# Optimization experiments

Measured on AMD Instinct MI355X. Metric: run time of the kernel, lower is better.

The kernel has to match this reference:

```python
import jax, jax.numpy as jnp
import numpy as np

B, S, F = 512, 512, 128   # batch, seq_len, facts_size (= querry_size)
H1, H2 = 80, 40
PAD = float(-2**32 + 1)


def setup_inputs() -> dict:
    key = jax.random.key(0)
    ks = jax.random.split(key, 12)
    inp = {
        "query": jax.random.normal(ks[0], (B, F), jnp.float32),
        "facts": jax.random.normal(ks[1], (B, S, F), jnp.float32),
        "mask": jax.random.randint(ks[2], (B, S), 0, 2, jnp.int32),
        # mlp1: querry_size -> facts_size
        "W1": jax.random.normal(ks[3], (F, F), jnp.float32) / np.sqrt(F),
        "b1": jnp.zeros((F,), jnp.float32),
        # PReLU alpha (per-feature, init zeros)
        "alpha": jnp.zeros((F,), jnp.float32),
        # mlp2: 4*F -> 80
        "W2": jax.random.normal(ks[4], (4 * F, H1), jnp.float32) / np.sqrt(4 * F),
        "b2": jnp.zeros((H1,), jnp.float32),
        # mlp3: 80 -> 40
        "W3": jax.random.normal(ks[5], (H1, H2), jnp.float32) / np.sqrt(H1),
        "b3": jnp.zeros((H2,), jnp.float32),
        # mlp4: 40 -> 1
        "W4": jax.random.normal(ks[6], (H2, 1), jnp.float32) / np.sqrt(H2),
        "b4": jnp.zeros((1,), jnp.float32),
    }
    return inp


def reference(query, facts, mask, W1, b1, alpha, W2, b2, W3, b3, W4, b4):
    # mlp1 + PReLU on the query
    q = query @ W1 + b1                                   # [B, F]
    q = jnp.where(q >= 0, q, alpha * q)                   # PReLU, alpha per-feature
    # broadcast query over sequence (tile+reshape in the original)
    qs = jnp.broadcast_to(q[:, None, :], (q.shape[0], S, F))  # [B, S, F]
    din = jnp.concatenate([qs, facts, qs - facts, qs * facts], axis=-1)  # [B,S,4F]
    h1 = jax.nn.sigmoid(din @ W2 + b2)                    # [B, S, 80]
    h2 = jax.nn.sigmoid(h1 @ W3 + b3)                     # [B, S, 40]
    scores = (h2 @ W4 + b4)[..., 0][:, None, :]           # [B, 1, S]
    key_masks = (mask == 1)[:, None, :]                   # [B, 1, S]
    scores = jnp.where(key_masks, scores, PAD)
    scores = jax.nn.softmax(scores, axis=-1)              # softmax over seq
    out = jnp.einsum("bqs,bsf->bqf", scores, facts)       # [B, 1, F]  (mode SUM)
    return out
```

## Files before the change

kernel.cpp:

```cpp
#include <hip/hip_runtime.h>
#include <hip/hip_bf16.h>

typedef __bf16 bf16x8 __attribute__((ext_vector_type(8)));
typedef float  f32x4  __attribute__((ext_vector_type(4)));

#define WBT_STRIDE 136
#define H1_STRIDE  104
#define W3T_STRIDE 104

#define LOAD_TILE(av, tile)                                                     \
    {                                                                           \
        const float* p0 = &fb[(size_t)(wave * 64 + (tile) * 16 + m) * 128 + qd * 8]; \
        _Pragma("unroll")                                                       \
        for (int kc = 0; kc < 4; ++kc) {                                        \
            av[kc][0] = *(const f32x4*)(p0 + kc * 32);                          \
            av[kc][1] = *(const f32x4*)(p0 + kc * 32 + 4);                      \
        }                                                                       \
    }

#define TILE_BODY(av, mvv)                                                      \
    {                                                                           \
        bf16x8 af[4];                                                           \
        _Pragma("unroll")                                                       \
        for (int kc = 0; kc < 4; ++kc)                                          \
            _Pragma("unroll")                                                   \
            for (int i = 0; i < 8; ++i)                                         \
                af[kc][i] = (__bf16)((i < 4) ? av[kc][0][i] : av[kc][1][i - 4]);\
         \
        _Pragma("unroll")                                                       \
        for (int ct = 0; ct < 5; ++ct) {                                        \
            f32x4 acc = {0.f, 0.f, 0.f, 0.f};                                   \
            _Pragma("unroll")                                                   \
            for (int kc = 0; kc < 4; ++kc) {                                    \
                bf16x8 bfr = *(const bf16x8*)&WbT[(ct * 16 + m) * WBT_STRIDE + kc * 32 + qd * 8]; \
                acc = __builtin_amdgcn_mfma_f32_16x16x32_bf16(af[kc], bfr, acc, 0, 0, 0); \
            }                                                                   \
            const int col = ct * 16 + m;    \
            const float qc = qcs[col];                                          \
            _Pragma("unroll")                                                   \
            for (int r = 0; r < 4; ++r) {                                       \
                float x = acc[r] + qc;                                          \
                float h = __builtin_amdgcn_rcpf(1.0f + __expf(-x));             \
                h1w[(qd * 4 + r) * H1_STRIDE + col] = (__bf16)h;                \
            }                                                                   \
        }                                                                       \
        asm volatile("s_waitcnt lgkmcnt(0)" ::: "memory");    \
                      \
        bf16x8 a2[3];                                                           \
        _Pragma("unroll")                                                       \
        for (int kc = 0; kc < 3; ++kc)                                          \
            a2[kc] = *(const bf16x8*)&h1w[m * H1_STRIDE + kc * 32 + qd * 8];    \
        float sc[4] = {0.f, 0.f, 0.f, 0.f};                                     \
        _Pragma("unroll")                                                       \
        for (int ct = 0; ct < 3; ++ct) {                                        \
            f32x4 acc2 = {0.f, 0.f, 0.f, 0.f};                                  \
            _Pragma("unroll")                                                   \
            for (int kc = 0; kc < 3; ++kc) {                                    \
                bf16x8 bfr = *(const bf16x8*)&W3T[(ct * 16 + m) * W3T_STRIDE + kc * 32 + qd * 8]; \
                acc2 = __builtin_amdgcn_mfma_f32_16x16x32_bf16(a2[kc], bfr, acc2, 0, 0, 0); \
            }                                                                   \
            const int col = ct * 16 + m;                                        \
            const float w4v = w4s[col], b3v = b3s[col];                         \
            _Pragma("unroll")                                                   \
            for (int r = 0; r < 4; ++r) {                                       \
                float h2 = __builtin_amdgcn_rcpf(1.0f + __expf(-(acc2[r] + b3v))); \
                sc[r] = fmaf(h2, w4v, sc[r]);                                   \
            }                                                                   \
        }                                                                       \
        _Pragma("unroll")                                                       \
        for (int d = 1; d < 16; d <<= 1)                                        \
            _Pragma("unroll")                                                   \
            for (int r = 0; r < 4; ++r)                                         \
                sc[r] += __shfl_xor(sc[r], d);                                  \
          \
        float s0v = __int_as_float(__builtin_amdgcn_ds_bpermute(idx, __float_as_int(sc[0]))); \
        float s1v = __int_as_float(__builtin_amdgcn_ds_bpermute(idx, __float_as_int(sc[1]))); \
        float s2v = __int_as_float(__builtin_amdgcn_ds_bpermute(idx, __float_as_int(sc[2]))); \
        float s3v = __int_as_float(__builtin_amdgcn_ds_bpermute(idx, __float_as_int(sc[3]))); \
        const int rr = m & 3;                                                   \
        float srow = (rr == 0) ? s0v : (rr == 1) ? s1v : (rr == 2) ? s2v : s3v; \
               \
        const float pm = ((mvv) == 1) ? __expf(srow) : 0.f;                     \
        Zl += pm;                                                               \
        _Pragma("unroll")                                                       \
        for (int kc = 0; kc < 4; ++kc)                                          \
            _Pragma("unroll")                                                   \
            for (int i = 0; i < 4; ++i) {                                       \
                oacc[kc][i]     = fmaf(pm, av[kc][0][i], oacc[kc][i]);          \
                oacc[kc][i + 4] = fmaf(pm, av[kc][1][i], oacc[kc][i + 4]);      \
            }                                                                   \
    }

__global__ __launch_bounds__(512, 4)
void attn_fused(const float* __restrict__ query,
                const float* __restrict__ facts,
                const int*   __restrict__ mask,
                const float* __restrict__ W1, const float* __restrict__ b1,
                const float* __restrict__ alpha,
                const float* __restrict__ W2, const float* __restrict__ b2,
                const float* __restrict__ W3, const float* __restrict__ b3,
                const float* __restrict__ W4,
                float* __restrict__ out)
{
    __shared__ __align__(16) __bf16 WbT[80 * WBT_STRIDE];
    __shared__ __align__(16) __bf16 W3T[48 * W3T_STRIDE];
    __shared__ __align__(16) __bf16 h1all[128 * H1_STRIDE];
    __shared__ float qy[128], qs[128], qcs[80];
    __shared__ float qpart[4][128], qcp[4][80];
    __shared__ float w4s[48], b3s[48];
    __shared__ float outw[8 * 128];
    __shared__ float Zw[8];

    const int b = blockIdx.x, t = threadIdx.x;
    const int wave = t >> 6, lane = t & 63, qd = lane >> 4, m = lane & 15;
    const float* fb = facts + (size_t)b * (512 * 128);
    const int*   mb = mask + b * 512;

    f32x4 av0[4][2], av1[4][2];
    LOAD_TILE(av0, 0)
    LOAD_TILE(av1, 1)
    const int mv0 = mb[wave * 64 + m];
    const int mv1 = mb[wave * 64 + 16 + m];
    const int mv2 = mb[wave * 64 + 32 + m];
    const int mv3 = mb[wave * 64 + 48 + m];

    if (t < 128) qy[t] = query[b * 128 + t];
    for (int e = t; e < 48 * 96; e += 512) {
        int j = e / 96, k = e % 96;
        W3T[j * W3T_STRIDE + k] = (j < 40 && k < 80) ? (__bf16)W3[k * 40 + j]
                                                     : (__bf16)0.0f;
    }
    for (int e = t; e < 128 * 16; e += 512) {
        int r = e >> 4, c = 80 + (e & 15);
        h1all[r * H1_STRIDE + c] = (__bf16)0.0f;
    }
    if (t < 48) { w4s[t] = (t < 40) ? W4[t] : 0.f; b3s[t] = (t < 40) ? b3[t] : 0.f; }
    __syncthreads();

    {
        int j = t & 127, kh = t >> 7;
        float acc = (kh == 0) ? b1[j] : 0.f;
        const float* w1p = W1 + (kh * 32) * 128 + j;
        #pragma unroll 8
        for (int k = 0; k < 32; ++k) acc = fmaf(qy[kh * 32 + k], w1p[k * 128], acc);
        qpart[kh][j] = acc;
    }
    __syncthreads();
    if (t < 128) {
        float s = (qpart[0][t] + qpart[1][t]) + (qpart[2][t] + qpart[3][t]);
        qs[t] = (s >= 0.f) ? s : alpha[t] * s;
    }
    __syncthreads();

    if (t < 320) {
        int jj = t % 80, hh = t / 80;
        float acc = (hh == 0) ? b2[jj] : 0.f;
        #pragma unroll 8
        for (int k = hh * 32; k < hh * 32 + 32; ++k)
            acc = fmaf(qs[k], W2[k * 80 + jj] + W2[(256 + k) * 80 + jj], acc);
        qcp[hh][jj] = acc;
    }
    for (int e = t; e < 128 * 80; e += 512) {
        int k = e / 80, n = e - k * 80;
        float w = W2[(128 + k) * 80 + n] - W2[(256 + k) * 80 + n]
                + qs[k] * W2[(384 + k) * 80 + n];
        WbT[n * WBT_STRIDE + k] = (__bf16)w;
    }
    __syncthreads();
    if (t < 80) qcs[t] = (qcp[0][t] + qcp[1][t]) + (qcp[2][t] + qcp[3][t]);
    __syncthreads();

    __bf16* h1w = &h1all[wave * 16 * H1_STRIDE];
    const int idx = ((((m >> 2) << 4) | m) << 2);

    float oacc[4][8];
    #pragma unroll
    for (int kc = 0; kc < 4; ++kc)
        #pragma unroll
        for (int i = 0; i < 8; ++i) oacc[kc][i] = 0.f;
    float Zl = 0.f;

    TILE_BODY(av0, mv0)
    LOAD_TILE(av0, 2)
    TILE_BODY(av1, mv1)
    LOAD_TILE(av1, 3)
    TILE_BODY(av0, mv2)
    TILE_BODY(av1, mv3)

    #pragma unroll
    for (int d = 1; d < 16; d <<= 1) {
        #pragma unroll
        for (int kc = 0; kc < 4; ++kc)
            #pragma unroll
            for (int i = 0; i < 8; ++i)
                oacc[kc][i] += __shfl_xor(oacc[kc][i], d);
        Zl += __shfl_xor(Zl, d);
    }
    if (m == 0) {
        #pragma unroll
        for (int kc = 0; kc < 4; ++kc)
            #pragma unroll
            for (int i = 0; i < 8; ++i)
                outw[wave * 128 + kc * 32 + qd * 8 + i] = oacc[kc][i];
        if (lane == 0) Zw[wave] = Zl;
    }
    __syncthreads();

    if (t < 128) {
        float v = 0.f, Z = 0.f;
        #pragma unroll
        for (int w = 0; w < 8; ++w) { v += outw[w * 128 + t]; Z += Zw[w]; }
        out[b * 128 + t] = v / Z;
    }
}

extern "C" void kernel_launch(void* const* d_in, const int* in_sizes, int n_in,
                              void* d_out, int out_size, void* d_ws, size_t ws_size,
                              hipStream_t stream) {
    (void)in_sizes; (void)n_in; (void)d_ws; (void)ws_size; (void)out_size;
    const float* query = (const float*)d_in[0];
    const float* facts = (const float*)d_in[1];
    const int*   mask  = (const int*)d_in[2];
    const float* W1 = (const float*)d_in[3];
    const float* b1 = (const float*)d_in[4];
    const float* al = (const float*)d_in[5];
    const float* W2 = (const float*)d_in[6];
    const float* b2 = (const float*)d_in[7];
    const float* W3 = (const float*)d_in[8];
    const float* b3 = (const float*)d_in[9];
    const float* W4 = (const float*)d_in[10];
    const float* b4 = (const float*)d_in[11];
    (void)b4;
    attn_fused<<<dim3(512), dim3(512), 0, stream>>>(
        query, facts, mask, W1, b1, al, W2, b2, W3, b3, W4, (float*)d_out);
}
```

Before: 259.5 us.

## Split score computation from weighted accumulation to cut live registers

Each tile's fp32 facts are converted to bf16 and the scores are computed right away, before the output accumulators exist. All four tiles are then re-read from global memory in a second pass that does the weighted sum. This keeps the 32 oacc registers out of the MLP/MFMA phase so register pressure drops there, in exchange for loading the facts tiles twice (second read likely from cache).

```diff
diff --git a/kernel.cpp b/kernel.cpp
--- a/kernel.cpp
+++ b/kernel.cpp
@@ -18,14 +18,15 @@
         }                                                                       \
     }
 
-#define TILE_BODY(av, mvv)                                                      \
+#define CONV_AF(af, av)                                                         \
+    _Pragma("unroll")                                                           \
+    for (int kc = 0; kc < 4; ++kc)                                              \
+        _Pragma("unroll")                                                       \
+        for (int i = 0; i < 8; ++i)                                             \
+            af[kc][i] = (__bf16)((i < 4) ? av[kc][0][i] : av[kc][1][i - 4]);
+
+#define SCORE_TILE(af, mvv, pmv)                                                \
     {                                                                           \
-        bf16x8 af[4];                                                           \
-        _Pragma("unroll")                                                       \
-        for (int kc = 0; kc < 4; ++kc)                                          \
-            _Pragma("unroll")                                                   \
-            for (int i = 0; i < 8; ++i)                                         \
-                af[kc][i] = (__bf16)((i < 4) ? av[kc][0][i] : av[kc][1][i - 4]);\
          \
         _Pragma("unroll")                                                       \
         for (int ct = 0; ct < 5; ++ct) {                                        \
@@ -80,16 +81,18 @@
         const int rr = m & 3;                                                   \
         float srow = (rr == 0) ? s0v : (rr == 1) ? s1v : (rr == 2) ? s2v : s3v; \
                \
-        const float pm = ((mvv) == 1) ? __expf(srow) : 0.f;                     \
-        Zl += pm;                                                               \
-        _Pragma("unroll")                                                       \
-        for (int kc = 0; kc < 4; ++kc)                                          \
-            _Pragma("unroll")                                                   \
-            for (int i = 0; i < 4; ++i) {                                       \
-                oacc[kc][i]     = fmaf(pm, av[kc][0][i], oacc[kc][i]);          \
-                oacc[kc][i + 4] = fmaf(pm, av[kc][1][i], oacc[kc][i + 4]);      \
-            }                                                                   \
-    }
+        pmv = ((mvv) == 1) ? __expf(srow) : 0.f;                                \
+        Zl += pmv;                                                              \
+    }
+
+#define ACC_TILE(bv, pmv)                                                       \
+    _Pragma("unroll")                                                           \
+    for (int kc = 0; kc < 4; ++kc)                                              \
+        _Pragma("unroll")                                                       \
+        for (int i = 0; i < 4; ++i) {                                           \
+            oacc[kc][i]     = fmaf(pmv, bv[kc][0][i], oacc[kc][i]);             \
+            oacc[kc][i + 4] = fmaf(pmv, bv[kc][1][i], oacc[kc][i + 4]);         \
+        }
 
 __global__ __launch_bounds__(512, 4)
 void attn_fused(const float* __restrict__ query,
@@ -173,19 +176,38 @@
     __bf16* h1w = &h1all[wave * 16 * H1_STRIDE];
     const int idx = ((((m >> 2) << 4) | m) << 2);
 
+    float Zl = 0.f;
+    float pm0, pm1, pm2, pm3;
+    bf16x8 af[4];
+
+    CONV_AF(af, av0)
+    LOAD_TILE(av0, 2)
+    SCORE_TILE(af, mv0, pm0)
+
+    CONV_AF(af, av1)
+    LOAD_TILE(av1, 3)
+    SCORE_TILE(af, mv1, pm1)
+
+    CONV_AF(af, av0)
+    SCORE_TILE(af, mv2, pm2)
+
+    CONV_AF(af, av1)
+    SCORE_TILE(af, mv3, pm3)
+
     float oacc[4][8];
     #pragma unroll
     for (int kc = 0; kc < 4; ++kc)
         #pragma unroll
         for (int i = 0; i < 8; ++i) oacc[kc][i] = 0.f;
-    float Zl = 0.f;
-
-    TILE_BODY(av0, mv0)
+
+    LOAD_TILE(av0, 0)
+    LOAD_TILE(av1, 1)
+    ACC_TILE(av0, pm0)
     LOAD_TILE(av0, 2)
-    TILE_BODY(av1, mv1)
+    ACC_TILE(av1, pm1)
     LOAD_TILE(av1, 3)
-    TILE_BODY(av0, mv2)
-    TILE_BODY(av1, mv3)
+    ACC_TILE(av0, pm2)
+    ACC_TILE(av1, pm3)
 
     #pragma unroll
     for (int d = 1; d < 16; d <<= 1) {
```

After: 249.8 us. -3.7%, faster.

## Stage softmax weights in LDS and re-read facts for weighted sum

Applied to the files above, without the earlier changes.

Each tile now stores only its per-row softmax numerators in shared memory instead of accumulating a 32-float weighted-sum register array per lane. After scoring, each wave re-reads its 64 fact rows from global memory (L2 cache) with coalesced lane-per-column loads and accumulates the output directly. This removes the large cross-lane shuffle reduction of the output. Double-buffered register tiles are replaced by a single buffer that is prefetched one tile ahead, and the launch bound is relaxed to 2 blocks per CU. The aim is to cut register pressure and shuffle cost, at the price of a second pass over facts through cache and possibly lower occupancy.

```diff
diff --git a/kernel.cpp b/kernel.cpp
--- a/kernel.cpp
+++ b/kernel.cpp
@@ -18,14 +18,15 @@
         }                                                                       \
     }
 
-#define TILE_BODY(av, mvv)                                                      \
+#define CONV_AF(af, av)                                                         \
+    _Pragma("unroll")                                                           \
+    for (int kc = 0; kc < 4; ++kc)                                              \
+        _Pragma("unroll")                                                       \
+        for (int i = 0; i < 8; ++i)                                             \
+            af[kc][i] = (__bf16)((i < 4) ? av[kc][0][i] : av[kc][1][i - 4]);
+
+#define SCORE_TILE(af, mvv, tile)                                               \
     {                                                                           \
-        bf16x8 af[4];                                                           \
-        _Pragma("unroll")                                                       \
-        for (int kc = 0; kc < 4; ++kc)                                          \
-            _Pragma("unroll")                                                   \
-            for (int i = 0; i < 8; ++i)                                         \
-                af[kc][i] = (__bf16)((i < 4) ? av[kc][0][i] : av[kc][1][i - 4]);\
          \
         _Pragma("unroll")                                                       \
         for (int ct = 0; ct < 5; ++ct) {                                        \
@@ -80,18 +81,12 @@
         const int rr = m & 3;                                                   \
         float srow = (rr == 0) ? s0v : (rr == 1) ? s1v : (rr == 2) ? s2v : s3v; \
                \
-        const float pm = ((mvv) == 1) ? __expf(srow) : 0.f;                     \
-        Zl += pm;                                                               \
-        _Pragma("unroll")                                                       \
-        for (int kc = 0; kc < 4; ++kc)                                          \
-            _Pragma("unroll")                                                   \
-            for (int i = 0; i < 4; ++i) {                                       \
-                oacc[kc][i]     = fmaf(pm, av[kc][0][i], oacc[kc][i]);          \
-                oacc[kc][i + 4] = fmaf(pm, av[kc][1][i], oacc[kc][i + 4]);      \
-            }                                                                   \
-    }
-
-__global__ __launch_bounds__(512, 4)
+        const float pmv = ((mvv) == 1) ? __expf(srow) : 0.f;                    \
+        Zl += pmv;                                                              \
+        if (qd == 0) pmall[wave * 64 + (tile) * 16 + m] = pmv;                  \
+    }
+
+__global__ __launch_bounds__(512, 2)
 void attn_fused(const float* __restrict__ query,
                 const float* __restrict__ facts,
                 const int*   __restrict__ mask,
@@ -109,6 +104,7 @@
     __shared__ float qpart[4][128], qcp[4][80];
     __shared__ float w4s[48], b3s[48];
     __shared__ float outw[8 * 128];
+    __shared__ float pmall[8 * 64];
     __shared__ float Zw[8];
 
     const int b = blockIdx.x, t = threadIdx.x;
@@ -116,9 +112,8 @@
     const float* fb = facts + (size_t)b * (512 * 128);
     const int*   mb = mask + b * 512;
 
-    f32x4 av0[4][2], av1[4][2];
-    LOAD_TILE(av0, 0)
-    LOAD_TILE(av1, 1)
+    f32x4 av[4][2];
+    LOAD_TILE(av, 0)
     const int mv0 = mb[wave * 64 + m];
     const int mv1 = mb[wave * 64 + 16 + m];
     const int mv2 = mb[wave * 64 + 32 + m];
@@ -173,37 +168,42 @@
     __bf16* h1w = &h1all[wave * 16 * H1_STRIDE];
     const int idx = ((((m >> 2) << 4) | m) << 2);
 
-    float oacc[4][8];
+    float Zl = 0.f;
+    bf16x8 af[4];
+
+    CONV_AF(af, av)
+    LOAD_TILE(av, 1)
+    SCORE_TILE(af, mv0, 0)
+
+    CONV_AF(af, av)
+    LOAD_TILE(av, 2)
+    SCORE_TILE(af, mv1, 1)
+
+    CONV_AF(af, av)
+    LOAD_TILE(av, 3)
+    SCORE_TILE(af, mv2, 2)
+
+    CONV_AF(af, av)
+    SCORE_TILE(af, mv3, 3)
+
+    asm volatile("s_waitcnt lgkmcnt(0)" ::: "memory");
+    float oA = 0.f, oB = 0.f;
+    {
+        const float* fw = fb + (size_t)(wave * 64) * 128;
+        const float* pmw = &pmall[wave * 64];
+        #pragma unroll 8
+        for (int s = 0; s < 64; ++s) {
+            const float p = pmw[s];
+            oA = fmaf(p, fw[s * 128 + lane], oA);
+            oB = fmaf(p, fw[s * 128 + 64 + lane], oB);
+        }
+        outw[wave * 128 + lane] = oA;
+        outw[wave * 128 + 64 + lane] = oB;
+    }
+
     #pragma unroll
-    for (int kc = 0; kc < 4; ++kc)
-        #pragma unroll
-        for (int i = 0; i < 8; ++i) oacc[kc][i] = 0.f;
-    float Zl = 0.f;
-
-    TILE_BODY(av0, mv0)
-    LOAD_TILE(av0, 2)
-    TILE_BODY(av1, mv1)
-    LOAD_TILE(av1, 3)
-    TILE_BODY(av0, mv2)
-    TILE_BODY(av1, mv3)
-
-    #pragma unroll
-    for (int d = 1; d < 16; d <<= 1) {
-        #pragma unroll
-        for (int kc = 0; kc < 4; ++kc)
-            #pragma unroll
-            for (int i = 0; i < 8; ++i)
-                oacc[kc][i] += __shfl_xor(oacc[kc][i], d);
-        Zl += __shfl_xor(Zl, d);
-    }
-    if (m == 0) {
-        #pragma unroll
-        for (int kc = 0; kc < 4; ++kc)
-            #pragma unroll
-            for (int i = 0; i < 8; ++i)
-                outw[wave * 128 + kc * 32 + qd * 8 + i] = oacc[kc][i];
-        if (lane == 0) Zw[wave] = Zl;
-    }
+    for (int d = 1; d < 16; d <<= 1) Zl += __shfl_xor(Zl, d);
+    if (lane == 0) Zw[wave] = Zl;
     __syncthreads();
 
     if (t < 128) {
```

Result: faster. 228.4 us (-12.0%).
